# Kernel optimization log

Hardware: AMD Instinct MI355X
Metric: run time of the kernel (lower is better)

## Reference

```python
import jax, jax.numpy as jnp
import numpy as np

B, S, H, NH = 2, 2048, 1024, 16
HD = H // NH  # 64


def setup_inputs() -> dict:
    key = jax.random.key(0)
    ks = jax.random.split(key, 9)
    s = 1.0 / np.sqrt(H)
    d = {"x": jax.random.normal(ks[0], (B, S, H), jnp.float32)}
    for i, n in enumerate(["Wq", "Wk", "Wv", "Wo"]):
        d[n] = jax.random.normal(ks[1 + i], (H, H), jnp.float32) * s
    for i, n in enumerate(["bq", "bk", "bv", "bo"]):
        d[n] = jax.random.normal(ks[5 + i], (H,), jnp.float32) * s
    return d


def _heads(x, W, b):
    # torch nn.Linear: y = x @ W.T + b, then split heads -> (B, NH, S, HD)
    y = x @ W.T + b
    return y.reshape(B, S, NH, HD).transpose(0, 2, 1, 3)


def _tetra_channels(t):
    # tetrapoint vector [a, 1-a, a*(1-a), clamp(1-(a+(1-a)),0,1)] for a scalar slice t
    a = jax.nn.sigmoid(t)
    na = 1.0 - a
    neither = jnp.clip(1.0 - (a + na), 0.0, 1.0)
    return jnp.stack([a, na, a * na, neither], axis=-1)  # (..., 4)


def reference(x, Wq, bq, Wk, bk, Wv, bv, Wo, bo):
    Q = _heads(x, Wq, bq)  # (B, NH, S, HD)
    K = _heads(x, Wk, bk)
    V = _heads(x, Wv, bv)
    # Original indexes Q_tetrapoints[:, :, :, 0] on [B,NH,S,HD,4]: selects head-dim
    # slot 0 (resp. 2) and keeps the 4 tetrapoint channels -> (B, NH, S, 4).
    Qa = _tetra_channels(Q[..., 0])
    Ka = _tetra_channels(K[..., 0])
    Qb = _tetra_channels(Q[..., 2])
    Kb = _tetra_channels(K[..., 2])
    scores = (jnp.einsum('bhsc,bhtc->bhst', Qa, Ka) / np.sqrt(HD)
              + 0.1 * jnp.einsum('bhsc,bhtc->bhst', Qb, Kb))  # (B, NH, S, S)
    w = jax.nn.softmax(scores, axis=-1)
    out = jnp.einsum('bhst,bhtd->bhsd', w, V)  # (B, NH, S, HD)
    out = out.transpose(0, 2, 1, 3).reshape(B, S, H)
    return out @ Wo.T + bo
```

## Files before the change

### kernel.cpp

```cpp
#include <hip/hip_runtime.h>
#include <hip/hip_bf16.h>

#define SS 2048
#define HH 1024
#define NHH 16
#define HDD 64

using f32x4  = __attribute__((ext_vector_type(4))) float;
using bf16x8 = __attribute__((ext_vector_type(8))) short;

#if __has_builtin(__builtin_amdgcn_exp2f)
#define EXP2F __builtin_amdgcn_exp2f
#else
#define EXP2F exp2f
#endif

__device__ __forceinline__ unsigned short f2bf(float f) {
    unsigned u = __builtin_bit_cast(unsigned, f);
    unsigned r = u + 0x7FFFu + ((u >> 16) & 1u);
    return (unsigned short)(r >> 16);
}

__device__ __forceinline__ unsigned bfround(float f) {
    unsigned u = __builtin_bit_cast(unsigned, f);
    return u + 0x7FFFu + ((u >> 16) & 1u);
}
__device__ __forceinline__ unsigned pack2bf(float a, float b) {
    return __builtin_amdgcn_perm(bfround(b), bfround(a), 0x07060302u);
}
__device__ __forceinline__ unsigned pack2bf_trunc(float a, float b) {
    return __builtin_amdgcn_perm(__builtin_bit_cast(unsigned, b),
                                 __builtin_bit_cast(unsigned, a), 0x07060302u);
}

__device__ __forceinline__ void tetra(float t, float* c) {
    float a = 1.f / (1.f + __expf(-t));
    float na = 1.f - a;
    float nei = 1.f - (a + na);
    nei = fminf(fmaxf(nei, 0.f), 1.f);
    c[0] = a; c[1] = na; c[2] = a * na; c[3] = nei;
}

__global__ __launch_bounds__(256) void cvt_kernel(
    const float* __restrict__ x, const float* __restrict__ Wv, const float* __restrict__ Wo,
    const float* __restrict__ Wq, const float* __restrict__ Wk,
    const float* __restrict__ bq, const float* __restrict__ bk,
    unsigned short* __restrict__ xb, unsigned short* __restrict__ Wvb, unsigned short* __restrict__ Wob,
    unsigned short* __restrict__ wselb, float* __restrict__ bselws)
{
    if (blockIdx.x >= 2048) {
        int n = blockIdx.x - 2048;
        int h = n >> 2, q = n & 3;
        int rowIdx = h * HDD + ((q & 1) ? 2 : 0);
        const float* src  = (q & 2) ? Wk : Wq;
        const float* bsrc = (q & 2) ? bk : bq;
        int t = threadIdx.x;
        float4 v = *(const float4*)(src + (size_t)rowIdx * HH + t * 4);
        uint2 pk;
        pk.x = pack2bf(v.x, v.y);
        pk.y = pack2bf(v.z, v.w);
        *(uint2*)(wselb + (size_t)n * HH + t * 4) = pk;
        if (t == 0) bselws[n] = bsrc[rowIdx];
        return;
    }
    size_t gid = (size_t)blockIdx.x * 256 + threadIdx.x;
    size_t base = gid * 8;
    {
        float4 a = *(const float4*)(x + base);
        float4 b = *(const float4*)(x + base + 4);
        uint4 pk;
        pk.x = pack2bf(a.x, a.y);
        pk.y = pack2bf(a.z, a.w);
        pk.z = pack2bf(b.x, b.y);
        pk.w = pack2bf(b.z, b.w);
        *(uint4*)(xb + base) = pk;
    }
    if (base < 1048576) {
        float4 a = *(const float4*)(Wv + base);
        float4 b = *(const float4*)(Wv + base + 4);
        uint4 pk;
        pk.x = pack2bf(a.x, a.y);
        pk.y = pack2bf(a.z, a.w);
        pk.z = pack2bf(b.x, b.y);
        pk.w = pack2bf(b.z, b.w);
        *(uint4*)(Wvb + base) = pk;
        a = *(const float4*)(Wo + base);
        b = *(const float4*)(Wo + base + 4);
        pk.x = pack2bf(a.x, a.y);
        pk.y = pack2bf(a.z, a.w);
        pk.z = pack2bf(b.x, b.y);
        pk.w = pack2bf(b.z, b.w);
        *(uint4*)(Wob + base) = pk;
    }
}

template<int OUT_MODE>
__device__ __forceinline__ void gemm_body(unsigned char* smem,
    const unsigned short* __restrict__ A, const unsigned short* __restrict__ Bw,
    const float* __restrict__ bias, void* __restrict__ Cout, int bx, int by)
{
    auto As = (unsigned short (*)[72])smem;
    auto Bs = (unsigned short (*)[72])(smem + 18432);
    int tid = threadIdx.x;
    int wave = tid >> 6, lane = tid & 63;
    int l15 = lane & 15, l16 = lane >> 4;
    int wm = wave >> 1, wn = wave & 1;
    int m0 = by * 128, n0 = bx * 64;

    int ar = tid >> 1, aseg = (tid & 1) * 32;
    int br = tid >> 2, bseg = (tid & 3) * 16;
    const unsigned short* Ap = A + (size_t)(m0 + ar) * HH + aseg;
    const unsigned short* Bp = Bw + (size_t)(n0 + br) * HH + bseg;

    f32x4 acc[4][2] = {};

    uint4 a0 = *(const uint4*)(Ap);
    uint4 a1 = *(const uint4*)(Ap + 8);
    uint4 a2 = *(const uint4*)(Ap + 16);
    uint4 a3 = *(const uint4*)(Ap + 24);
    uint4 b0 = *(const uint4*)(Bp);
    uint4 b1 = *(const uint4*)(Bp + 8);

    for (int k0 = 0; k0 < HH; k0 += 64) {
        __syncthreads();
        *(uint4*)&As[ar][aseg]      = a0;
        *(uint4*)&As[ar][aseg + 8]  = a1;
        *(uint4*)&As[ar][aseg + 16] = a2;
        *(uint4*)&As[ar][aseg + 24] = a3;
        *(uint4*)&Bs[br][bseg]      = b0;
        *(uint4*)&Bs[br][bseg + 8]  = b1;
        __syncthreads();

        int kn = (k0 + 64) & (HH - 1);
        uint4 na0 = *(const uint4*)(Ap + kn);
        uint4 na1 = *(const uint4*)(Ap + kn + 8);
        uint4 na2 = *(const uint4*)(Ap + kn + 16);
        uint4 na3 = *(const uint4*)(Ap + kn + 24);
        uint4 nb0 = *(const uint4*)(Bp + kn);
        uint4 nb1 = *(const uint4*)(Bp + kn + 8);

        #pragma unroll
        for (int kk = 0; kk < 64; kk += 32) {
            bf16x8 af[4], bfr[2];
            #pragma unroll
            for (int mi = 0; mi < 4; mi++)
                af[mi] = *(const bf16x8*)&As[wm * 64 + mi * 16 + l15][kk + l16 * 8];
            #pragma unroll
            for (int ni = 0; ni < 2; ni++)
                bfr[ni] = *(const bf16x8*)&Bs[wn * 32 + ni * 16 + l15][kk + l16 * 8];
            #pragma unroll
            for (int mi = 0; mi < 4; mi++)
                #pragma unroll
                for (int ni = 0; ni < 2; ni++)
                    acc[mi][ni] = __builtin_amdgcn_mfma_f32_16x16x32_bf16(af[mi], bfr[ni], acc[mi][ni], 0, 0, 0);
        }
        a0 = na0; a1 = na1; a2 = na2; a3 = na3; b0 = nb0; b1 = nb1;
    }

    float bv[2];
    #pragma unroll
    for (int ni = 0; ni < 2; ni++)
        bv[ni] = bias[n0 + wn * 32 + ni * 16 + l15];

    #pragma unroll
    for (int mi = 0; mi < 4; mi++) {
        #pragma unroll
        for (int ni = 0; ni < 2; ni++) {
            int n = n0 + wn * 32 + ni * 16 + l15;
            if (OUT_MODE == 0) {
                #pragma unroll
                for (int r = 0; r < 4; r++) {
                    int m = m0 + wm * 64 + mi * 16 + l16 * 4 + r;
                    ((float*)Cout)[(size_t)m * HH + n] = acc[mi][ni][r] + bv[ni];
                }
            } else {
                int m = m0 + wm * 64 + mi * 16 + l16 * 4;
                int b = m >> 11, s = m & 2047;
                int h = n >> 6, d = n & 63;
                uint2 pk;
                pk.x = pack2bf(acc[mi][ni][0] + bv[ni], acc[mi][ni][1] + bv[ni]);
                pk.y = pack2bf(acc[mi][ni][2] + bv[ni], acc[mi][ni][3] + bv[ni]);
                *(uint2*)((unsigned short*)Cout + ((size_t)((b * NHH + h) * HDD + d)) * SS + s) = pk;
            }
        }
    }
}

__device__ __forceinline__ void qk_body(unsigned char* smem,
    const unsigned short* __restrict__ xb, const unsigned short* __restrict__ wselb,
    const float* __restrict__ bselws,
    unsigned short* __restrict__ qfb, unsigned short* __restrict__ kfb, int blk)
{
    auto xs = (unsigned short (*)[72])smem;
    auto ws = (unsigned short (*)[72])(smem + 4608);
    auto ys = (float (*)[68])(smem + 13824);
    int tid = threadIdx.x;
    int wave = tid >> 6, lane = tid & 63;
    int l15 = lane & 15, l16 = lane >> 4;
    int m0 = blk * 32;
    int n0w = wave * 16;

    int xr = tid >> 3, xseg = (tid & 7) * 8;
    int wr = tid >> 2, wseg = (tid & 3) * 16;
    const unsigned short* xp = xb + (size_t)(m0 + xr) * HH + xseg;
    const unsigned short* wp = wselb + (size_t)wr * HH + wseg;

    f32x4 acc[2] = {};

    uint4 xv  = *(const uint4*)(xp);
    uint4 wv0 = *(const uint4*)(wp);
    uint4 wv1 = *(const uint4*)(wp + 8);

    for (int k0 = 0; k0 < HH; k0 += 64) {
        __syncthreads();
        *(uint4*)&xs[xr][xseg] = xv;
        *(uint4*)&ws[wr][wseg]     = wv0;
        *(uint4*)&ws[wr][wseg + 8] = wv1;
        __syncthreads();

        int kn = (k0 + 64) & (HH - 1);
        uint4 nxv  = *(const uint4*)(xp + kn);
        uint4 nwv0 = *(const uint4*)(wp + kn);
        uint4 nwv1 = *(const uint4*)(wp + kn + 8);

        #pragma unroll
        for (int kk = 0; kk < 64; kk += 32) {
            bf16x8 bfr = *(const bf16x8*)&ws[n0w + l15][kk + l16 * 8];
            #pragma unroll
            for (int mi = 0; mi < 2; mi++) {
                bf16x8 af = *(const bf16x8*)&xs[mi * 16 + l15][kk + l16 * 8];
                acc[mi] = __builtin_amdgcn_mfma_f32_16x16x32_bf16(af, bfr, acc[mi], 0, 0, 0);
            }
        }
        xv = nxv; wv0 = nwv0; wv1 = nwv1;
    }

    float bias = bselws[n0w + l15];
    __syncthreads();
    #pragma unroll
    for (int mi = 0; mi < 2; mi++)
        #pragma unroll
        for (int r = 0; r < 4; r++)
            ys[mi * 16 + l16 * 4 + r][n0w + l15] = acc[mi][r] + bias;
    __syncthreads();

    #pragma unroll
    for (int pass = 0; pass < 2; pass++) {
        int ml = tid & 31;
        int h = (tid >> 5) + pass * 8;
        float4 y4 = *(const float4*)&ys[ml][h * 4];
        float qa[4], qb2[4], ka[4], kb2[4];
        tetra(y4.x, qa);
        tetra(y4.y, qb2);
        tetra(y4.z, ka);
        tetra(y4.w, kb2);
        int m = m0 + ml, b = m >> 11, s = m & 2047;
        size_t base = ((size_t)(b * NHH + h) * SS + s) * 8;
        const float sA = 0.18033688011112042f;
        const float sB = 0.14426950408889634f;
        uint4 qp, kp;
        qp.x = pack2bf(qa[0] * sA, qa[1] * sA);
        qp.y = pack2bf(qa[2] * sA, qa[3] * sA);
        qp.z = pack2bf(qb2[0] * sB, qb2[1] * sB);
        qp.w = pack2bf(qb2[2] * sB, qb2[3] * sB);
        kp.x = pack2bf(ka[0], ka[1]);
        kp.y = pack2bf(ka[2], ka[3]);
        kp.z = pack2bf(kb2[0], kb2[1]);
        kp.w = pack2bf(kb2[2], kb2[3]);
        *(uint4*)(qfb + base) = qp;
        *(uint4*)(kfb + base) = kp;
    }
}

__global__ __launch_bounds__(256) void fused_mid(
    const unsigned short* __restrict__ xb,
    const unsigned short* __restrict__ Wvb, const float* __restrict__ bv,
    unsigned short* __restrict__ Vt,
    const unsigned short* __restrict__ wselb, const float* __restrict__ bselws,
    unsigned short* __restrict__ qfb, unsigned short* __restrict__ kfb)
{
    __shared__ __align__(16) unsigned char smem[27648];
    int id = blockIdx.x;
    if (id < 512)
        gemm_body<2>(smem, xb, Wvb, bv, Vt, id & 15, id >> 4);
    else
        qk_body(smem, xb, wselb, bselws, qfb, kfb, id - 512);
}

__global__ __launch_bounds__(256) void gemm_out(
    const unsigned short* __restrict__ A, const unsigned short* __restrict__ Bw,
    const float* __restrict__ bias, float* __restrict__ Cout)
{
    __shared__ __align__(16) unsigned char smem[27648];
    gemm_body<0>(smem, A, Bw, bias, Cout, blockIdx.x, blockIdx.y);
}

__global__ __launch_bounds__(256) void attn_mfma(
    const unsigned short* __restrict__ qfb, const unsigned short* __restrict__ kfb,
    const unsigned short* __restrict__ Vt, unsigned short* __restrict__ attnb)
{
    __shared__ __align__(16) unsigned char lds[32768];

    int tid = threadIdx.x;
    int wave = tid >> 6, lane = tid & 63;
    int l15 = lane & 15, l16 = lane >> 4;
    int l7 = l15 & 7;

    int L = blockIdx.x + (blockIdx.y << 4);
    int logical = ((L & 7) << 6) + (L >> 3);
    int bh = logical >> 4, qblk = logical & 15;
    int b = bh >> 4, h = bh & 15;
    int s0 = qblk * 128 + wave * 32;

    bf16x8 qA = {0,0,0,0,0,0,0,0}, qB = {0,0,0,0,0,0,0,0};
    if (l16 == 0) {
        qA = *(const bf16x8*)(qfb + ((size_t)bh * SS + s0 + l15) * 8);
        qB = *(const bf16x8*)(qfb + ((size_t)bh * SS + s0 + 16 + l15) * 8);
    }

    const short oneb = 0x3F80;
    bf16x8 ones = {oneb,oneb,oneb,oneb,oneb,oneb,oneb,oneb};

    const unsigned short* kfA = kfb + ((size_t)bh * SS + l15) * 8;
    int vd = tid >> 2, vr = tid & 3;
    const unsigned short* vsrc = Vt + ((size_t)bh * HDD + vd) * SS + vr * 16;

    unsigned char* vrow = lds + vd * 128;
    int sw0 = ((vr * 2)     ^ (vd & 7)) << 4;
    int sw1 = ((vr * 2 + 1) ^ (vd & 7)) << 4;
    unsigned char* psw = lds + 16384 + wave * 4096;

    f32x4 acc[2][4] = {};
    f32x4 accl[2] = {};

    {
        uint4 t0a = *(const uint4*)(vsrc);
        uint4 t0b = *(const uint4*)(vsrc + 8);
        *(uint4*)(vrow + sw0) = t0a;
        *(uint4*)(vrow + sw1) = t0b;
    }
    uint4 sv0 = *(const uint4*)(vsrc + 64);
    uint4 sv1 = *(const uint4*)(vsrc + 64 + 8);
    bf16x8 kfr[4];
    #pragma unroll
    for (int tb = 0; tb < 4; tb++)
        kfr[tb] = *(const bf16x8*)(kfA + (size_t)(tb * 16) * 8);

    for (int it = 0; it < 32; it++) {
        int t0 = it << 6;
        __syncthreads();

        int nb = (it + 1) & 1;
        *(uint4*)(vrow + nb * 8192 + sw0) = sv0;
        *(uint4*)(vrow + nb * 8192 + sw1) = sv1;

        int tv = (t0 + 128) & (SS - 1);
        uint4 nv0 = *(const uint4*)(vsrc + tv);
        uint4 nv1 = *(const uint4*)(vsrc + tv + 8);
        int tkf = (t0 + 64) & (SS - 1);
        bf16x8 nkf[4];
        #pragma unroll
        for (int tb = 0; tb < 4; tb++)
            nkf[tb] = *(const bf16x8*)(kfA + (size_t)(tkf + tb * 16) * 8);

        #pragma unroll
        for (int g = 0; g < 2; g++) {
            bf16x8 qf = g ? qB : qA;
            #pragma unroll
            for (int tb = 0; tb < 4; tb++) {
                f32x4 sc = {};
                sc = __builtin_amdgcn_mfma_f32_16x16x32_bf16(kfr[tb], qf, sc, 0, 0, 0);
                uint2 pw;
                pw.x = pack2bf_trunc(EXP2F(sc[0]), EXP2F(sc[1]));
                pw.y = pack2bf_trunc(EXP2F(sc[2]), EXP2F(sc[3]));
                int qr = g * 16 + l15;
                int c  = (tb * 2 + (l16 >> 1)) ^ l7;
                *(uint2*)(psw + qr * 128 + c * 16 + (l16 & 1) * 8) = pw;
            }
        }

        int cb = it & 1;
        unsigned char* vbuf = lds + cb * 8192;
        __builtin_amdgcn_s_setprio(1);
        #pragma unroll
        for (int tk = 0; tk < 2; tk++) {
            int csw = ((tk * 4 + l16) ^ l7) << 4;
            bf16x8 apA = *(const bf16x8*)(psw + l15 * 128 + csw);
            bf16x8 apB = *(const bf16x8*)(psw + (16 + l15) * 128 + csw);
            accl[0] = __builtin_amdgcn_mfma_f32_16x16x32_bf16(apA, ones, accl[0], 0, 0, 0);
            accl[1] = __builtin_amdgcn_mfma_f32_16x16x32_bf16(apB, ones, accl[1], 0, 0, 0);
            #pragma unroll
            for (int nd = 0; nd < 4; nd++) {
                bf16x8 bv = *(const bf16x8*)(vbuf + (nd * 16 + l15) * 128 + csw);
                acc[0][nd] = __builtin_amdgcn_mfma_f32_16x16x32_bf16(apA, bv, acc[0][nd], 0, 0, 0);
                acc[1][nd] = __builtin_amdgcn_mfma_f32_16x16x32_bf16(apB, bv, acc[1][nd], 0, 0, 0);
            }
        }
        __builtin_amdgcn_s_setprio(0);

        sv0 = nv0; sv1 = nv1;
        #pragma unroll
        for (int tb = 0; tb < 4; tb++) kfr[tb] = nkf[tb];
    }

    #pragma unroll
    for (int g = 0; g < 2; g++) {
        #pragma unroll
        for (int r = 0; r < 4; r++) {
            float linv = 1.f / accl[g][r];
            int q = s0 + g * 16 + l16 * 4 + r;
            size_t row = (size_t)(b * SS + q) * HH + h * HDD;
            #pragma unroll
            for (int nd = 0; nd < 4; nd++)
                attnb[row + nd * 16 + l15] = f2bf(acc[g][nd][r] * linv);
        }
    }
}

extern "C" void kernel_launch(void* const* d_in, const int* in_sizes, int n_in,
                              void* d_out, int out_size, void* d_ws, size_t ws_size,
                              hipStream_t stream)
{
    const float* x  = (const float*)d_in[0];
    const float* Wq = (const float*)d_in[1];
    const float* Wk = (const float*)d_in[2];
    const float* Wv = (const float*)d_in[3];
    const float* Wo = (const float*)d_in[4];
    const float* bq = (const float*)d_in[5];
    const float* bk = (const float*)d_in[6];
    const float* bv = (const float*)d_in[7];
    const float* bo = (const float*)d_in[8];

    unsigned short* qfb   = (unsigned short*)d_ws;
    unsigned short* kfb   = qfb + 524288;
    unsigned short* xb    = kfb + 524288;
    unsigned short* attnb = xb;
    unsigned short* Wvb   = xb + 4194304;
    unsigned short* Wob   = Wvb + 1048576;
    unsigned short* Vt    = Wob + 1048576;
    unsigned short* wselb  = Vt + 4194304;
    float*          bselws = (float*)(wselb + 65536);

    cvt_kernel<<<2112, 256, 0, stream>>>(x, Wv, Wo, Wq, Wk, bq, bk, xb, Wvb, Wob, wselb, bselws);
    fused_mid<<<640, 256, 0, stream>>>(xb, Wvb, bv, Vt, wselb, bselws, qfb, kfb);
    attn_mfma<<<dim3(16, 32), 256, 0, stream>>>(qfb, kfb, Vt, attnb);
    gemm_out<<<dim3(16, 32), 256, 0, stream>>>(attnb, Wob, bo, (float*)d_out);
}
```

Before: 169.0 us.

## Load GEMM tiles directly into LDS with global_load_lds, dropping register staging

```diff
diff --git a/kernel.cpp b/kernel.cpp
--- a/kernel.cpp
+++ b/kernel.cpp
@@ -39,6 +39,12 @@
     float nei = 1.f - (a + na);
     nei = fminf(fmaxf(nei, 0.f), 1.f);
     c[0] = a; c[1] = na; c[2] = a * na; c[3] = nei;
+}
+
+__device__ __forceinline__ void gll16(const unsigned short* g, unsigned short* l) {
+    __builtin_amdgcn_global_load_lds(
+        (const __attribute__((address_space(1))) unsigned int*)g,
+        (__attribute__((address_space(3))) unsigned int*)l, 16, 0, 0);
 }
 
 __global__ __launch_bounds__(256) void cvt_kernel(
@@ -99,45 +105,31 @@
     const unsigned short* __restrict__ A, const unsigned short* __restrict__ Bw,
     const float* __restrict__ bias, void* __restrict__ Cout, int bx, int by)
 {
-    auto As = (unsigned short (*)[72])smem;
-    auto Bs = (unsigned short (*)[72])(smem + 18432);
+    auto As = (unsigned short (*)[64])smem;
+    auto Bs = (unsigned short (*)[64])(smem + 16384);
     int tid = threadIdx.x;
     int wave = tid >> 6, lane = tid & 63;
     int l15 = lane & 15, l16 = lane >> 4;
     int wm = wave >> 1, wn = wave & 1;
     int m0 = by * 128, n0 = bx * 64;
 
-    int ar = tid >> 1, aseg = (tid & 1) * 32;
-    int br = tid >> 2, bseg = (tid & 3) * 16;
-    const unsigned short* Ap = A + (size_t)(m0 + ar) * HH + aseg;
-    const unsigned short* Bp = Bw + (size_t)(n0 + br) * HH + bseg;
+    int srow = tid >> 3, scol = (tid & 7) * 8;
+    const unsigned short* Ag = A + (size_t)(m0 + srow) * HH + scol;
+    const unsigned short* Bg = Bw + (size_t)(n0 + srow) * HH + scol;
+    unsigned short* Asl = &As[srow][scol];
+    unsigned short* Bsl = &Bs[srow][scol];
 
     f32x4 acc[4][2] = {};
-
-    uint4 a0 = *(const uint4*)(Ap);
-    uint4 a1 = *(const uint4*)(Ap + 8);
-    uint4 a2 = *(const uint4*)(Ap + 16);
-    uint4 a3 = *(const uint4*)(Ap + 24);
-    uint4 b0 = *(const uint4*)(Bp);
-    uint4 b1 = *(const uint4*)(Bp + 8);
 
     for (int k0 = 0; k0 < HH; k0 += 64) {
         __syncthreads();
-        *(uint4*)&As[ar][aseg]      = a0;
-        *(uint4*)&As[ar][aseg + 8]  = a1;
-        *(uint4*)&As[ar][aseg + 16] = a2;
-        *(uint4*)&As[ar][aseg + 24] = a3;
-        *(uint4*)&Bs[br][bseg]      = b0;
-        *(uint4*)&Bs[br][bseg + 8]  = b1;
+        #pragma unroll
+        for (int i = 0; i < 4; i++)
+            gll16(Ag + (size_t)(i * 32) * HH + k0, Asl + i * 32 * 64);
+        #pragma unroll
+        for (int i = 0; i < 2; i++)
+            gll16(Bg + (size_t)(i * 32) * HH + k0, Bsl + i * 32 * 64);
         __syncthreads();
-
-        int kn = (k0 + 64) & (HH - 1);
-        uint4 na0 = *(const uint4*)(Ap + kn);
-        uint4 na1 = *(const uint4*)(Ap + kn + 8);
-        uint4 na2 = *(const uint4*)(Ap + kn + 16);
-        uint4 na3 = *(const uint4*)(Ap + kn + 24);
-        uint4 nb0 = *(const uint4*)(Bp + kn);
-        uint4 nb1 = *(const uint4*)(Bp + kn + 8);
 
         #pragma unroll
         for (int kk = 0; kk < 64; kk += 32) {
@@ -154,7 +146,6 @@
                 for (int ni = 0; ni < 2; ni++)
                     acc[mi][ni] = __builtin_amdgcn_mfma_f32_16x16x32_bf16(af[mi], bfr[ni], acc[mi][ni], 0, 0, 0);
         }
-        a0 = na0; a1 = na1; a2 = na2; a3 = na3; b0 = nb0; b1 = nb1;
     }
 
     float bv[2];
@@ -279,7 +270,7 @@
     const unsigned short* __restrict__ wselb, const float* __restrict__ bselws,
     unsigned short* __restrict__ qfb, unsigned short* __restrict__ kfb)
 {
-    __shared__ __align__(16) unsigned char smem[27648];
+    __shared__ __align__(16) unsigned char smem[24576];
     int id = blockIdx.x;
     if (id < 512)
         gemm_body<2>(smem, xb, Wvb, bv, Vt, id & 15, id >> 4);
@@ -291,7 +282,7 @@
     const unsigned short* __restrict__ A, const unsigned short* __restrict__ Bw,
     const float* __restrict__ bias, float* __restrict__ Cout)
 {
-    __shared__ __align__(16) unsigned char smem[27648];
+    __shared__ __align__(16) unsigned char smem[24576];
     gemm_body<0>(smem, A, Bw, bias, Cout, blockIdx.x, blockIdx.y);
 }
 
```

Result: slower. 173.4 us (+2.6%).
